# Kernel tuning notes

Measured on AMD Instinct MI355X. Metric: run time of the kernel, lower is better.

The kernel has to match this reference:

```python
import jax, jax.numpy as jnp
import numpy as np

N = 50000        # nodes
F_IN = 128       # input features
HID = 128        # hidden_size
H = 4            # heads
C = HID // H     # per-head channels (32)
E_RAND = 800000  # random edges; + N self loops -> E = 850000
NEG_SLOPE = 0.2  # PyG GATConv default leaky_relu slope


def setup_inputs() -> dict:
    key = jax.random.key(0)
    ks = jax.random.split(key, 12)
    x = jax.random.normal(ks[0], (N, F_IN), jnp.float32)
    src_r = jax.random.randint(ks[1], (E_RAND,), 0, N)
    dst_r = jax.random.randint(ks[2], (E_RAND,), 0, N)
    loops = jnp.arange(N)
    src = jnp.concatenate([src_r, loops]).astype(jnp.int32)
    dst = jnp.concatenate([dst_r, loops]).astype(jnp.int32)

    def glorot(k, shape):
        fan_in, fan_out = shape[0], shape[-1]
        lim = np.sqrt(6.0 / (fan_in + fan_out)).astype(np.float32)
        return jax.random.uniform(k, shape, jnp.float32, -lim, lim)

    return {
        "x": x, "src": src, "dst": dst,
        "W0": glorot(ks[3], (F_IN, HID)),
        "a_src0": glorot(ks[4], (H, C)),
        "a_dst0": glorot(ks[5], (H, C)),
        "b0": jnp.zeros((HID,), jnp.float32),
        "W1": glorot(ks[6], (HID, HID)),
        "a_src1": glorot(ks[7], (H, C)),
        "a_dst1": glorot(ks[8], (H, C)),
        "b1": jnp.zeros((HID,), jnp.float32),
    }


def gat_layer(x, W, a_src, a_dst, b, src, dst):
    # linear projection -> [N, H, C]
    xp = (x @ W).reshape(-1, H, C)
    # per-node attention logits [N, H]
    al_src = jnp.einsum("nhc,hc->nh", xp, a_src)
    al_dst = jnp.einsum("nhc,hc->nh", xp, a_dst)
    # edge logits [E, H]
    e = jax.nn.leaky_relu(al_src[src] + al_dst[dst], NEG_SLOPE)
    # scatter softmax over incoming edges of each destination node
    m = jax.ops.segment_max(e, dst, num_segments=N)
    p = jnp.exp(e - m[dst])
    s = jax.ops.segment_sum(p, dst, num_segments=N)
    alpha = p / (s[dst] + 1e-16)
    # weighted message aggregation: [E, H, C] scatter-add -> [N, H, C]
    out = jax.ops.segment_sum(xp[src] * alpha[:, :, None], dst, num_segments=N)
    return out.reshape(-1, H * C) + b  # concat heads + bias


def reference(x, src, dst, W0, a_src0, a_dst0, b0, W1, a_src1, a_dst1, b1):
    h = jax.nn.relu(gat_layer(x, W0, a_src0, a_dst0, b0, src, dst))
    h = jax.nn.relu(gat_layer(h, W1, a_src1, a_dst1, b1, src, dst))
    return h
```

## Files before the change

### kernel.cpp

```cpp
#include <hip/hip_runtime.h>
#include <math.h>

#define NEG_SLOPE 0.2f
#define BCAP 4096
#define TILE 4096

using short8 = __attribute__((ext_vector_type(8))) short;
using f32x4 = __attribute__((ext_vector_type(4))) float;

__device__ __forceinline__ float leaky(float x) { return x > 0.f ? x : NEG_SLOPE * x; }

__device__ __forceinline__ float wmax64(float v) {
#pragma unroll
  for (int off = 32; off; off >>= 1) v = fmaxf(v, __shfl_xor(v, off));
  return v;
}
__device__ __forceinline__ float wsum64(float v) {
#pragma unroll
  for (int off = 32; off; off >>= 1) v += __shfl_xor(v, off);
  return v;
}

__device__ __forceinline__ unsigned short f2bf(float f) {
  union { float f; unsigned u; } x; x.f = f;
  unsigned r = x.u + 0x7fff + ((x.u >> 16) & 1);
  return (unsigned short)(r >> 16);
}
__device__ __forceinline__ float bf2f(unsigned short h) {
  union { unsigned u; float f; } x; x.u = (unsigned)h << 16;
  return x.f;
}

__device__ __forceinline__ void acc8(float* a, float p, uint4 rv) {
  a[0] += p * __uint_as_float(rv.x << 16);
  a[1] += p * __uint_as_float(rv.x & 0xffff0000u);
  a[2] += p * __uint_as_float(rv.y << 16);
  a[3] += p * __uint_as_float(rv.y & 0xffff0000u);
  a[4] += p * __uint_as_float(rv.z << 16);
  a[5] += p * __uint_as_float(rv.z & 0xffff0000u);
  a[6] += p * __uint_as_float(rv.w << 16);
  a[7] += p * __uint_as_float(rv.w & 0xffff0000u);
}

__global__ __launch_bounds__(256) void k_hist_wsplit(
    const int* __restrict__ dst, int* __restrict__ blkhist, int E, int nb, int nblk,
    const float* __restrict__ W0, const float* __restrict__ W1,
    unsigned short* __restrict__ Wth0, unsigned short* __restrict__ Wtl0,
    unsigned short* __restrict__ Wth1, unsigned short* __restrict__ Wtl1) {
  __shared__ int h[512];
  if (blockIdx.x < 128) {
    int i = blockIdx.x * 256 + threadIdx.x;
    int j = i & 16383;
    int k = j >> 7, n = j & 127;
    const float* W = (i < 16384) ? W0 : W1;
    float v = W[j];
    unsigned short hi = f2bf(v);
    unsigned short lo = f2bf(v - bf2f(hi));
    if (i < 16384) {
      Wth0[n * 128 + k] = hi;
      Wtl0[n * 128 + k] = lo;
    } else {
      Wth1[n * 128 + k] = hi;
      Wtl1[n * 128 + k] = lo;
    }
    return;
  }
  int blk = blockIdx.x - 128;
  for (int i = threadIdx.x; i < nb; i += 256) h[i] = 0;
  __syncthreads();
  int t0 = blk * TILE;
  int end = t0 + TILE < E ? t0 + TILE : E;
  for (int i = t0 + threadIdx.x; i < end; i += 256) atomicAdd(&h[dst[i] >> 7], 1);
  __syncthreads();
  for (int i = threadIdx.x; i < nb; i += 256) blkhist[(size_t)i * nblk + blk] = h[i];
}

__global__ __launch_bounds__(256) void k_bofs(int* __restrict__ blkhist,
                                              int* __restrict__ btot, int nblk) {
  __shared__ int sd[256];
  int b = blockIdx.x, t = threadIdx.x;
  int v = (t < nblk) ? blkhist[(size_t)b * nblk + t] : 0;
  sd[t] = v;
  __syncthreads();
  for (int off = 1; off < 256; off <<= 1) {
    int add = (t >= off) ? sd[t - off] : 0;
    __syncthreads();
    sd[t] += add;
    __syncthreads();
  }
  if (t < nblk) blkhist[(size_t)b * nblk + t] = sd[t] - v;
  if (t == 255) btot[b] = sd[255];
}

__global__ __launch_bounds__(256) void k_scatter2(
    const int* __restrict__ src, const int* __restrict__ dst,
    const int* __restrict__ blkhist, const int* __restrict__ btot,
    int2* __restrict__ bstore, int E, int nb, int nblk) {
  __shared__ int sd[256];
  __shared__ int bb[512];
  __shared__ int cur[512];
  int t = threadIdx.x, blk = blockIdx.x;
  int v0 = (2 * t < nb) ? btot[2 * t] : 0;
  int v1 = (2 * t + 1 < nb) ? btot[2 * t + 1] : 0;
  int s = v0 + v1;
  sd[t] = s;
  __syncthreads();
  for (int off = 1; off < 256; off <<= 1) {
    int add = (t >= off) ? sd[t - off] : 0;
    __syncthreads();
    sd[t] += add;
    __syncthreads();
  }
  int run = sd[t] - s;
  if (2 * t < nb) bb[2 * t] = run;
  if (2 * t + 1 < nb) bb[2 * t + 1] = run + v0;
  __syncthreads();
  for (int i = t; i < nb; i += 256)
    cur[i] = bb[i] + blkhist[(size_t)i * nblk + blk];
  __syncthreads();
  int t0 = blk * TILE;
  int end = t0 + TILE < E ? t0 + TILE : E;
  for (int i = t0 + t; i < end; i += 256) {
    int d = dst[i];
    int pos = atomicAdd(&cur[d >> 7], 1);
    bstore[pos] = make_int2(src[i], d);
  }
}

__global__ __launch_bounds__(256) void k_build(
    const int2* __restrict__ bstore, const int* __restrict__ btot,
    int* __restrict__ ssrc, int* __restrict__ deg, int* __restrict__ rstart, int N) {
  __shared__ int ls[BCAP];
  __shared__ unsigned char lloc[BCAP];
  __shared__ int lout[BCAP];
  __shared__ int hist[128];
  __shared__ int sc[128];
  __shared__ int lcur[128];
  __shared__ int red[256];
  int b = blockIdx.x;
  int t = threadIdx.x;
  int pacc = 0;
  for (int j = t; j < b; j += 256) pacc += btot[j];
  red[t] = pacc;
  __syncthreads();
  for (int off = 128; off; off >>= 1) {
    if (t < off) red[t] += red[t + off];
    __syncthreads();
  }
  int base = red[0];
  int cnt = btot[b];
  if (cnt > BCAP) cnt = BCAP;
  int nlo = b << 7;
  if (t < 128) { hist[t] = 0; lcur[t] = 0; }
  __syncthreads();
  for (int i = t; i < cnt; i += 256) {
    int2 e = bstore[base + i];
    int loc = e.y - nlo;
    ls[i] = e.x;
    lloc[i] = (unsigned char)loc;
    atomicAdd(&hist[loc], 1);
  }
  __syncthreads();
  int hv = (t < 128) ? hist[t] : 0;
  if (t < 128) sc[t] = hv;
  __syncthreads();
  for (int off = 1; off < 128; off <<= 1) {
    int add = (t < 128 && t >= off) ? sc[t - off] : 0;
    __syncthreads();
    if (t < 128) sc[t] += add;
    __syncthreads();
  }
  int lstart = (t < 128) ? sc[t] - hv : 0;
  if (t < 128) sc[t] = lstart;
  if (t < 128 && nlo + t < N) {
    deg[nlo + t] = hv;
    rstart[nlo + t] = base + lstart;
  }
  __syncthreads();
  for (int i = t; i < cnt; i += 256) {
    int loc = lloc[i];
    int slot = sc[loc] + atomicAdd(&lcur[loc], 1);
    lout[slot] = ls[i];
  }
  __syncthreads();
  for (int i = t; i < cnt; i += 256) ssrc[base + i] = lout[i];
}

#define PA 136
#define PW 40
__global__ __launch_bounds__(256, 2) void k_gemm_mfma(
    const float* __restrict__ A, const unsigned short* __restrict__ Wth,
    const unsigned short* __restrict__ Wtl, const float* __restrict__ a_src,
    const float* __restrict__ a_dst, unsigned short* __restrict__ xph,
    float* __restrict__ als, float* __restrict__ ald, int nrows) {
  __shared__ unsigned short Ah[64 * PA];
  __shared__ unsigned short Al[64 * PA];
  __shared__ unsigned short Wh[128 * PW];
  __shared__ unsigned short Wl[128 * PW];
  int t = threadIdx.x;
  int row0 = blockIdx.x * 64;

  const float4* A4 = (const float4*)A;
#pragma unroll
  for (int p = 0; p < 8; ++p) {
    int idx = t + p * 256;
    int row = idx >> 5, k4 = idx & 31;
    int gr = row0 + row;
    float4 v = make_float4(0.f, 0.f, 0.f, 0.f);
    if (gr < nrows) v = A4[(size_t)gr * 32 + k4];
    ushort4 hi, lo;
    hi.x = f2bf(v.x); lo.x = f2bf(v.x - bf2f(hi.x));
    hi.y = f2bf(v.y); lo.y = f2bf(v.y - bf2f(hi.y));
    hi.z = f2bf(v.z); lo.z = f2bf(v.z - bf2f(hi.z));
    hi.w = f2bf(v.w); lo.w = f2bf(v.w - bf2f(hi.w));
    *(ushort4*)&Ah[row * PA + k4 * 4] = hi;
    *(ushort4*)&Al[row * PA + k4 * 4] = lo;
  }

  int lane = t & 63, wv = t >> 6;
  int wr = wv >> 1, wc = wv & 1;
  int ml = lane & 15, q = lane >> 4;
  f32x4 acc[2][4] = {};

  for (int kb = 0; kb < 4; ++kb) {
    __syncthreads();
    int k0 = kb * 32;
#pragma unroll
    for (int p = 0; p < 8; ++p) {
      int idx = t + p * 256;
      int n = idx >> 4, kp = idx & 15;
      *(unsigned*)&Wh[n * PW + kp * 2] =
          *(const unsigned*)(Wth + (size_t)n * 128 + k0 + kp * 2);
      *(unsigned*)&Wl[n * PW + kp * 2] =
          *(const unsigned*)(Wtl + (size_t)n * 128 + k0 + kp * 2);
    }
    __syncthreads();
    int kf = k0 + q * 8;
    short8 a_h0 = *(const short8*)&Ah[(wr * 32 + ml) * PA + kf];
    short8 a_h1 = *(const short8*)&Ah[(wr * 32 + 16 + ml) * PA + kf];
    short8 a_l0 = *(const short8*)&Al[(wr * 32 + ml) * PA + kf];
    short8 a_l1 = *(const short8*)&Al[(wr * 32 + 16 + ml) * PA + kf];
#pragma unroll
    for (int ct = 0; ct < 4; ++ct) {
      int nb = (wc * 64 + ct * 16 + ml) * PW + q * 8;
      short8 b_h = *(const short8*)&Wh[nb];
      short8 b_l = *(const short8*)&Wl[nb];
      acc[0][ct] = __builtin_amdgcn_mfma_f32_16x16x32_bf16(a_h0, b_h, acc[0][ct], 0, 0, 0);
      acc[0][ct] = __builtin_amdgcn_mfma_f32_16x16x32_bf16(a_h0, b_l, acc[0][ct], 0, 0, 0);
      acc[0][ct] = __builtin_amdgcn_mfma_f32_16x16x32_bf16(a_l0, b_h, acc[0][ct], 0, 0, 0);
      acc[1][ct] = __builtin_amdgcn_mfma_f32_16x16x32_bf16(a_h1, b_h, acc[1][ct], 0, 0, 0);
      acc[1][ct] = __builtin_amdgcn_mfma_f32_16x16x32_bf16(a_h1, b_l, acc[1][ct], 0, 0, 0);
      acc[1][ct] = __builtin_amdgcn_mfma_f32_16x16x32_bf16(a_l1, b_h, acc[1][ct], 0, 0, 0);
    }
  }

  float asr[4], adr[4];
#pragma unroll
  for (int ct = 0; ct < 4; ++ct) {
    int col = (wc * 2 + (ct >> 1)) * 32 + (ct & 1) * 16 + ml;
    asr[ct] = a_src[col];
    adr[ct] = a_dst[col];
  }

#pragma unroll
  for (int rt = 0; rt < 2; ++rt) {
#pragma unroll
    for (int r = 0; r < 4; ++r) {
      int gr = row0 + wr * 32 + rt * 16 + q * 4 + r;
      bool valid = gr < nrows;
      if (valid) {
#pragma unroll
        for (int ct = 0; ct < 4; ++ct) {
          int gc = wc * 64 + ct * 16 + ml;
          xph[(size_t)gr * 128 + gc] = f2bf(acc[rt][ct][r]);
        }
      }
      float p0 = acc[rt][0][r] * asr[0] + acc[rt][1][r] * asr[1];
      float p1 = acc[rt][2][r] * asr[2] + acc[rt][3][r] * asr[3];
      float d0 = acc[rt][0][r] * adr[0] + acc[rt][1][r] * adr[1];
      float d1 = acc[rt][2][r] * adr[2] + acc[rt][3][r] * adr[3];
#pragma unroll
      for (int off = 1; off <= 8; off <<= 1) {
        p0 += __shfl_xor(p0, off); p1 += __shfl_xor(p1, off);
        d0 += __shfl_xor(d0, off); d1 += __shfl_xor(d1, off);
      }
      if (ml == 0 && valid) {
        als[(size_t)gr * 4 + wc * 2] = p0;
        als[(size_t)gr * 4 + wc * 2 + 1] = p1;
        ald[(size_t)gr * 4 + wc * 2] = d0;
        ald[(size_t)gr * 4 + wc * 2 + 1] = d1;
      }
    }
  }
}

__global__ __launch_bounds__(256) void k_aggregate(
    const unsigned short* __restrict__ xph, const float* __restrict__ als,
    const float* __restrict__ ald, const int* __restrict__ rstart,
    const int* __restrict__ deg, const int* __restrict__ ssrc,
    const float* __restrict__ bias, float* __restrict__ out, int N) {
  __shared__ float pbuf[4][128 * 4];
  __shared__ int snbuf[4][128];
  int wv = threadIdx.x >> 6;
  int lane = threadIdx.x & 63;
  int n = (blockIdx.x * blockDim.x + threadIdx.x) >> 6;
  if (n >= N) return;
  int start = rstart[n];
  int d = deg[n];
  float4 adv = *(const float4*)(ald + (size_t)n * 4);

  float m0, m1, m2, m3;
  float s0 = 0.f, s1 = 0.f, s2 = 0.f, s3 = 0.f;
  if (d <= 64) {
    int i = lane;
    bool valid = i < d;
    int sn = valid ? ssrc[start + i] : 0;
    if (valid) snbuf[wv][i] = sn;
    float4 av = *(const float4*)(als + (size_t)sn * 4);
    float L0 = valid ? leaky(av.x + adv.x) : -INFINITY;
    float L1 = valid ? leaky(av.y + adv.y) : -INFINITY;
    float L2 = valid ? leaky(av.z + adv.z) : -INFINITY;
    float L3 = valid ? leaky(av.w + adv.w) : -INFINITY;
    m0 = wmax64(L0); m1 = wmax64(L1); m2 = wmax64(L2); m3 = wmax64(L3);
    float p0 = __expf(L0 - m0);
    float p1 = __expf(L1 - m1);
    float p2 = __expf(L2 - m2);
    float p3 = __expf(L3 - m3);
    *(float4*)&pbuf[wv][lane * 4] = make_float4(p0, p1, p2, p3);
    s0 = wsum64(p0); s1 = wsum64(p1); s2 = wsum64(p2); s3 = wsum64(p3);
  } else {
    m0 = m1 = m2 = m3 = -INFINITY;
    for (int base = 0; base < d; base += 64) {
      int i = base + lane;
      bool valid = i < d;
      int sn = valid ? ssrc[start + i] : 0;
      if (valid) snbuf[wv][i] = sn;
      float4 av = *(const float4*)(als + (size_t)sn * 4);
      float L0 = valid ? leaky(av.x + adv.x) : -INFINITY;
      float L1 = valid ? leaky(av.y + adv.y) : -INFINITY;
      float L2 = valid ? leaky(av.z + adv.z) : -INFINITY;
      float L3 = valid ? leaky(av.w + adv.w) : -INFINITY;
      if (valid) *(float4*)&pbuf[wv][i * 4] = make_float4(L0, L1, L2, L3);
      m0 = fmaxf(m0, wmax64(L0)); m1 = fmaxf(m1, wmax64(L1));
      m2 = fmaxf(m2, wmax64(L2)); m3 = fmaxf(m3, wmax64(L3));
    }
    for (int base = 0; base < d; base += 64) {
      int i = base + lane;
      bool valid = i < d;
      float4 lv = valid ? *(const float4*)&pbuf[wv][i * 4]
                        : make_float4(-INFINITY, -INFINITY, -INFINITY, -INFINITY);
      float p0 = __expf(lv.x - m0), p1 = __expf(lv.y - m1);
      float p2 = __expf(lv.z - m2), p3 = __expf(lv.w - m3);
      if (valid) *(float4*)&pbuf[wv][i * 4] = make_float4(p0, p1, p2, p3);
      s0 += wsum64(p0); s1 += wsum64(p1); s2 += wsum64(p2); s3 += wsum64(p3);
    }
  }

  int cg = lane & 15;
  int es = lane >> 4;
  int c0 = cg * 8;
  int h = cg >> 2;
  float a[8] = {0.f, 0.f, 0.f, 0.f, 0.f, 0.f, 0.f, 0.f};
  int t = es;
  for (; t + 12 < d; t += 16) {
    int sn0 = snbuf[wv][t];
    int sn1 = snbuf[wv][t + 4];
    int sn2 = snbuf[wv][t + 8];
    int sn3 = snbuf[wv][t + 12];
    float q0 = pbuf[wv][t * 4 + h];
    float q1 = pbuf[wv][(t + 4) * 4 + h];
    float q2 = pbuf[wv][(t + 8) * 4 + h];
    float q3 = pbuf[wv][(t + 12) * 4 + h];
    uint4 r0 = *(const uint4*)(xph + (size_t)sn0 * 128 + c0);
    uint4 r1 = *(const uint4*)(xph + (size_t)sn1 * 128 + c0);
    uint4 r2 = *(const uint4*)(xph + (size_t)sn2 * 128 + c0);
    uint4 r3 = *(const uint4*)(xph + (size_t)sn3 * 128 + c0);
    acc8(a, q0, r0);
    acc8(a, q1, r1);
    acc8(a, q2, r2);
    acc8(a, q3, r3);
  }
  for (; t < d; t += 4) {
    int sn = snbuf[wv][t];
    float p = pbuf[wv][t * 4 + h];
    uint4 rv = *(const uint4*)(xph + (size_t)sn * 128 + c0);
    acc8(a, p, rv);
  }
#pragma unroll
  for (int off = 16; off <= 32; off <<= 1) {
#pragma unroll
    for (int j = 0; j < 8; ++j) a[j] += __shfl_xor(a[j], off);
  }
  if (es == 0) {
    float sden = h == 0 ? s0 : h == 1 ? s1 : h == 2 ? s2 : s3;
    float inv = 1.f / (sden + 1e-16f);
    float4 bv0 = *(const float4*)(bias + c0);
    float4 bv1 = *(const float4*)(bias + c0 + 4);
    float4 o0, o1;
    o0.x = fmaxf(a[0] * inv + bv0.x, 0.f);
    o0.y = fmaxf(a[1] * inv + bv0.y, 0.f);
    o0.z = fmaxf(a[2] * inv + bv0.z, 0.f);
    o0.w = fmaxf(a[3] * inv + bv0.w, 0.f);
    o1.x = fmaxf(a[4] * inv + bv1.x, 0.f);
    o1.y = fmaxf(a[5] * inv + bv1.y, 0.f);
    o1.z = fmaxf(a[6] * inv + bv1.z, 0.f);
    o1.w = fmaxf(a[7] * inv + bv1.w, 0.f);
    *(float4*)(out + (size_t)n * 128 + c0) = o0;
    *(float4*)(out + (size_t)n * 128 + c0 + 4) = o1;
  }
}

extern "C" void kernel_launch(void* const* d_in, const int* in_sizes, int n_in,
                              void* d_out, int out_size, void* d_ws, size_t ws_size,
                              hipStream_t stream) {
  const float* x   = (const float*)d_in[0];
  const int*   src = (const int*)d_in[1];
  const int*   dst = (const int*)d_in[2];
  const float* W0  = (const float*)d_in[3];
  const float* as0 = (const float*)d_in[4];
  const float* ad0 = (const float*)d_in[5];
  const float* b0  = (const float*)d_in[6];
  const float* W1  = (const float*)d_in[7];
  const float* as1 = (const float*)d_in[8];
  const float* ad1 = (const float*)d_in[9];
  const float* b1  = (const float*)d_in[10];
  float* out = (float*)d_out;

  int N = in_sizes[0] / 128;
  int E = in_sizes[1];
  int NB = (N + 127) >> 7;
  int NBLK = (E + TILE - 1) / TILE;

  char* w = (char*)d_ws;
  auto alloc = [&](size_t bytes) {
    char* p = w;
    w += (bytes + 255) & ~(size_t)255;
    return p;
  };
  int* deg     = (int*)alloc((size_t)N * 4);
  int* rstart  = (int*)alloc((size_t)N * 4);
  int* blkhist = (int*)alloc((size_t)NB * NBLK * 4);
  int* btot    = (int*)alloc((size_t)NB * 4);
  int2* bstore = (int2*)alloc((size_t)E * 8);
  int* ssrc    = (int*)alloc((size_t)E * 4);
  unsigned short* xph = (unsigned short*)alloc((size_t)N * 128 * 2);
  float* hbuf  = (float*)alloc((size_t)N * 128 * 4);
  float* als   = (float*)alloc((size_t)N * 4 * 4);
  float* ald   = (float*)alloc((size_t)N * 4 * 4);
  unsigned short* Wth0 = (unsigned short*)alloc(16384 * 2);
  unsigned short* Wtl0 = (unsigned short*)alloc(16384 * 2);
  unsigned short* Wth1 = (unsigned short*)alloc(16384 * 2);
  unsigned short* Wtl1 = (unsigned short*)alloc(16384 * 2);

  k_hist_wsplit<<<128 + NBLK, 256, 0, stream>>>(dst, blkhist, E, NB, NBLK,
                                                W0, W1, Wth0, Wtl0, Wth1, Wtl1);
  k_bofs<<<NB, 256, 0, stream>>>(blkhist, btot, NBLK);
  k_scatter2<<<NBLK, 256, 0, stream>>>(src, dst, blkhist, btot, bstore, E, NB, NBLK);
  k_build<<<NB, 256, 0, stream>>>(bstore, btot, ssrc, deg, rstart, N);

  int gb = (N + 63) / 64;
  k_gemm_mfma<<<gb, 256, 0, stream>>>(x, Wth0, Wtl0, as0, ad0, xph, als, ald, N);
  k_aggregate<<<(N + 3) / 4, 256, 0, stream>>>(xph, als, ald, rstart, deg, ssrc, b0, hbuf, N);

  k_gemm_mfma<<<gb, 256, 0, stream>>>(hbuf, Wth1, Wtl1, as1, ad1, xph, als, ald, N);
  k_aggregate<<<(N + 3) / 4, 256, 0, stream>>>(xph, als, ald, rstart, deg, ssrc, b1, out, N);
}
```

Measured before the change: 249.9 us.

## Split aggregation across heads: one wavefront per node-head pair

The aggregation kernel now launches four times as many blocks, each handling a single attention head for four nodes, instead of one wavefront processing all four heads of a node. Each wavefront computes a scalar softmax and gathers 32-channel slices (8 bytes per lane) rather than 128-channel rows. The aim is more parallelism and less per-wave register and shared-memory pressure. In exchange, the ssrc index, degree and row-start loads plus the softmax setup are repeated four times per node, and each gather moves narrower 64-byte segments.

```diff
diff --git a/kernel.cpp b/kernel.cpp
--- a/kernel.cpp
+++ b/kernel.cpp
@@ -29,17 +29,6 @@
 __device__ __forceinline__ float bf2f(unsigned short h) {
   union { unsigned u; float f; } x; x.u = (unsigned)h << 16;
   return x.f;
-}
-
-__device__ __forceinline__ void acc8(float* a, float p, uint4 rv) {
-  a[0] += p * __uint_as_float(rv.x << 16);
-  a[1] += p * __uint_as_float(rv.x & 0xffff0000u);
-  a[2] += p * __uint_as_float(rv.y << 16);
-  a[3] += p * __uint_as_float(rv.y & 0xffff0000u);
-  a[4] += p * __uint_as_float(rv.z << 16);
-  a[5] += p * __uint_as_float(rv.z & 0xffff0000u);
-  a[6] += p * __uint_as_float(rv.w << 16);
-  a[7] += p * __uint_as_float(rv.w & 0xffff0000u);
 }
 
 __global__ __launch_bounds__(256) void k_hist_wsplit(
@@ -298,115 +287,79 @@
     const unsigned short* __restrict__ xph, const float* __restrict__ als,
     const float* __restrict__ ald, const int* __restrict__ rstart,
     const int* __restrict__ deg, const int* __restrict__ ssrc,
-    const float* __restrict__ bias, float* __restrict__ out, int N) {
-  __shared__ float pbuf[4][128 * 4];
+    const float* __restrict__ bias, float* __restrict__ out, int N, int nbk) {
+  __shared__ float pbuf[4][128];
   __shared__ int snbuf[4][128];
   int wv = threadIdx.x >> 6;
   int lane = threadIdx.x & 63;
-  int n = (blockIdx.x * blockDim.x + threadIdx.x) >> 6;
+  int h = blockIdx.x / nbk;
+  int n = (blockIdx.x % nbk) * 4 + wv;
   if (n >= N) return;
   int start = rstart[n];
   int d = deg[n];
-  float4 adv = *(const float4*)(ald + (size_t)n * 4);
-
-  float m0, m1, m2, m3;
-  float s0 = 0.f, s1 = 0.f, s2 = 0.f, s3 = 0.f;
+  float adh = ald[(size_t)n * 4 + h];
+
+  float s;
   if (d <= 64) {
-    int i = lane;
-    bool valid = i < d;
-    int sn = valid ? ssrc[start + i] : 0;
-    if (valid) snbuf[wv][i] = sn;
-    float4 av = *(const float4*)(als + (size_t)sn * 4);
-    float L0 = valid ? leaky(av.x + adv.x) : -INFINITY;
-    float L1 = valid ? leaky(av.y + adv.y) : -INFINITY;
-    float L2 = valid ? leaky(av.z + adv.z) : -INFINITY;
-    float L3 = valid ? leaky(av.w + adv.w) : -INFINITY;
-    m0 = wmax64(L0); m1 = wmax64(L1); m2 = wmax64(L2); m3 = wmax64(L3);
-    float p0 = __expf(L0 - m0);
-    float p1 = __expf(L1 - m1);
-    float p2 = __expf(L2 - m2);
-    float p3 = __expf(L3 - m3);
-    *(float4*)&pbuf[wv][lane * 4] = make_float4(p0, p1, p2, p3);
-    s0 = wsum64(p0); s1 = wsum64(p1); s2 = wsum64(p2); s3 = wsum64(p3);
+    bool valid = lane < d;
+    int sn = valid ? ssrc[start + lane] : 0;
+    snbuf[wv][lane] = sn;
+    float av = als[(size_t)sn * 4 + h];
+    float L = valid ? leaky(av + adh) : -INFINITY;
+    float m = wmax64(L);
+    float p = __expf(L - m);
+    pbuf[wv][lane] = p;
+    s = wsum64(p);
   } else {
-    m0 = m1 = m2 = m3 = -INFINITY;
+    float m = -INFINITY;
     for (int base = 0; base < d; base += 64) {
       int i = base + lane;
       bool valid = i < d;
       int sn = valid ? ssrc[start + i] : 0;
       if (valid) snbuf[wv][i] = sn;
-      float4 av = *(const float4*)(als + (size_t)sn * 4);
-      float L0 = valid ? leaky(av.x + adv.x) : -INFINITY;
-      float L1 = valid ? leaky(av.y + adv.y) : -INFINITY;
-      float L2 = valid ? leaky(av.z + adv.z) : -INFINITY;
-      float L3 = valid ? leaky(av.w + adv.w) : -INFINITY;
-      if (valid) *(float4*)&pbuf[wv][i * 4] = make_float4(L0, L1, L2, L3);
-      m0 = fmaxf(m0, wmax64(L0)); m1 = fmaxf(m1, wmax64(L1));
-      m2 = fmaxf(m2, wmax64(L2)); m3 = fmaxf(m3, wmax64(L3));
-    }
+      float av = als[(size_t)sn * 4 + h];
+      float L = valid ? leaky(av + adh) : -INFINITY;
+      if (valid) pbuf[wv][i] = L;
+      m = fmaxf(m, wmax64(L));
+    }
+    s = 0.f;
     for (int base = 0; base < d; base += 64) {
       int i = base + lane;
       bool valid = i < d;
-      float4 lv = valid ? *(const float4*)&pbuf[wv][i * 4]
-                        : make_float4(-INFINITY, -INFINITY, -INFINITY, -INFINITY);
-      float p0 = __expf(lv.x - m0), p1 = __expf(lv.y - m1);
-      float p2 = __expf(lv.z - m2), p3 = __expf(lv.w - m3);
-      if (valid) *(float4*)&pbuf[wv][i * 4] = make_float4(p0, p1, p2, p3);
-      s0 += wsum64(p0); s1 += wsum64(p1); s2 += wsum64(p2); s3 += wsum64(p3);
-    }
-  }
-
-  int cg = lane & 15;
-  int es = lane >> 4;
-  int c0 = cg * 8;
-  int h = cg >> 2;
-  float a[8] = {0.f, 0.f, 0.f, 0.f, 0.f, 0.f, 0.f, 0.f};
-  int t = es;
-  for (; t + 12 < d; t += 16) {
-    int sn0 = snbuf[wv][t];
-    int sn1 = snbuf[wv][t + 4];
-    int sn2 = snbuf[wv][t + 8];
-    int sn3 = snbuf[wv][t + 12];
-    float q0 = pbuf[wv][t * 4 + h];
-    float q1 = pbuf[wv][(t + 4) * 4 + h];
-    float q2 = pbuf[wv][(t + 8) * 4 + h];
-    float q3 = pbuf[wv][(t + 12) * 4 + h];
-    uint4 r0 = *(const uint4*)(xph + (size_t)sn0 * 128 + c0);
-    uint4 r1 = *(const uint4*)(xph + (size_t)sn1 * 128 + c0);
-    uint4 r2 = *(const uint4*)(xph + (size_t)sn2 * 128 + c0);
-    uint4 r3 = *(const uint4*)(xph + (size_t)sn3 * 128 + c0);
-    acc8(a, q0, r0);
-    acc8(a, q1, r1);
-    acc8(a, q2, r2);
-    acc8(a, q3, r3);
-  }
-  for (; t < d; t += 4) {
+      float L = valid ? pbuf[wv][i] : -INFINITY;
+      float p = __expf(L - m);
+      if (valid) pbuf[wv][i] = p;
+      s += wsum64(p);
+    }
+  }
+
+  int es = lane >> 3;
+  int cg = lane & 7;
+  int c0 = h * 32 + cg * 4;
+  float a0 = 0.f, a1 = 0.f, a2 = 0.f, a3 = 0.f;
+  for (int t = es; t < d; t += 8) {
     int sn = snbuf[wv][t];
-    float p = pbuf[wv][t * 4 + h];
-    uint4 rv = *(const uint4*)(xph + (size_t)sn * 128 + c0);
-    acc8(a, p, rv);
-  }
-#pragma unroll
-  for (int off = 16; off <= 32; off <<= 1) {
-#pragma unroll
-    for (int j = 0; j < 8; ++j) a[j] += __shfl_xor(a[j], off);
+    float p = pbuf[wv][t];
+    uint2 rv = *(const uint2*)(xph + (size_t)sn * 128 + c0);
+    a0 += p * __uint_as_float(rv.x << 16);
+    a1 += p * __uint_as_float(rv.x & 0xffff0000u);
+    a2 += p * __uint_as_float(rv.y << 16);
+    a3 += p * __uint_as_float(rv.y & 0xffff0000u);
+  }
+#pragma unroll
+  for (int off = 8; off <= 32; off <<= 1) {
+    a0 += __shfl_xor(a0, off); a1 += __shfl_xor(a1, off);
+    a2 += __shfl_xor(a2, off); a3 += __shfl_xor(a3, off);
   }
   if (es == 0) {
-    float sden = h == 0 ? s0 : h == 1 ? s1 : h == 2 ? s2 : s3;
-    float inv = 1.f / (sden + 1e-16f);
-    float4 bv0 = *(const float4*)(bias + c0);
-    float4 bv1 = *(const float4*)(bias + c0 + 4);
-    float4 o0, o1;
-    o0.x = fmaxf(a[0] * inv + bv0.x, 0.f);
-    o0.y = fmaxf(a[1] * inv + bv0.y, 0.f);
-    o0.z = fmaxf(a[2] * inv + bv0.z, 0.f);
-    o0.w = fmaxf(a[3] * inv + bv0.w, 0.f);
-    o1.x = fmaxf(a[4] * inv + bv1.x, 0.f);
-    o1.y = fmaxf(a[5] * inv + bv1.y, 0.f);
-    o1.z = fmaxf(a[6] * inv + bv1.z, 0.f);
-    o1.w = fmaxf(a[7] * inv + bv1.w, 0.f);
-    *(float4*)(out + (size_t)n * 128 + c0) = o0;
-    *(float4*)(out + (size_t)n * 128 + c0 + 4) = o1;
+    float inv = 1.f / (s + 1e-16f);
+    float4 bv = *(const float4*)(bias + c0);
+    float4 o;
+    o.x = fmaxf(a0 * inv + bv.x, 0.f);
+    o.y = fmaxf(a1 * inv + bv.y, 0.f);
+    o.z = fmaxf(a2 * inv + bv.z, 0.f);
+    o.w = fmaxf(a3 * inv + bv.w, 0.f);
+    *(float4*)(out + (size_t)n * 128 + c0) = o;
   }
 }
 
@@ -459,9 +412,10 @@
   k_build<<<NB, 256, 0, stream>>>(bstore, btot, ssrc, deg, rstart, N);
 
   int gb = (N + 63) / 64;
+  int nbk = (N + 3) / 4;
   k_gemm_mfma<<<gb, 256, 0, stream>>>(x, Wth0, Wtl0, as0, ad0, xph, als, ald, N);
-  k_aggregate<<<(N + 3) / 4, 256, 0, stream>>>(xph, als, ald, rstart, deg, ssrc, b0, hbuf, N);
+  k_aggregate<<<4 * nbk, 256, 0, stream>>>(xph, als, ald, rstart, deg, ssrc, b0, hbuf, N, nbk);
 
   k_gemm_mfma<<<gb, 256, 0, stream>>>(hbuf, Wth1, Wtl1, as1, ad1, xph, als, ald, N);
-  k_aggregate<<<(N + 3) / 4, 256, 0, stream>>>(xph, als, ald, rstart, deg, ssrc, b1, out, N);
-}
+  k_aggregate<<<4 * nbk, 256, 0, stream>>>(xph, als, ald, rstart, deg, ssrc, b1, out, N, nbk);
+}
```

After: 356.9 us. 42.8% more time.
